# Kernel optimization log

Measured on AMD Instinct MI355X. Metric: run time of the kernel, lower is better.

Reference implementation:

```python
import jax, jax.numpy as jnp
import numpy as np

IN_DIM, HID_DIM, OUT_DIM = 768, 512, 256
B = 1024


def setup_inputs() -> dict:
    key = jax.random.key(0)
    ks = jax.random.split(key, 8)
    s = lambda fan_in: 1.0 / np.sqrt(fan_in)
    return {
        "combin_emb": jax.random.normal(ks[0], (B, IN_DIM), jnp.float32),
        "s_emb": jax.random.normal(ks[1], (B, HID_DIM), jnp.float32),
        # fn1: Linear(hid, hid); torch weight layout [out, in]
        "W1": jax.random.uniform(ks[2], (HID_DIM, HID_DIM), jnp.float32, -s(HID_DIM), s(HID_DIM)),
        "b1": jax.random.uniform(ks[3], (HID_DIM,), jnp.float32, -s(HID_DIM), s(HID_DIM)),
        # fn2: Linear(in, hid)
        "W2": jax.random.uniform(ks[4], (HID_DIM, IN_DIM), jnp.float32, -s(IN_DIM), s(IN_DIM)),
        "b2": jax.random.uniform(ks[5], (HID_DIM,), jnp.float32, -s(IN_DIM), s(IN_DIM)),
        # fn3: Linear(hid, out)
        "W3": jax.random.uniform(ks[6], (OUT_DIM, HID_DIM), jnp.float32, -s(HID_DIM), s(HID_DIM)),
        "b3": jax.random.uniform(ks[7], (OUT_DIM,), jnp.float32, -s(HID_DIM), s(HID_DIM)),
    }


def reference(combin_emb, s_emb, W1, b1, W2, b2, W3, b3):
    scale = 1.0 / np.sqrt(HID_DIM)
    c_emb = combin_emb @ W2.T + b2          # [B, H] query
    t_emb = s_emb @ W1.T + b1               # [B, H] key
    # outer-product scores: [B, H, H], softmax over key axis (last)
    scores = scale * c_emb[:, :, None] * t_emb[:, None, :]
    attn = jax.nn.softmax(scores, axis=-1)
    # value is raw s_emb: [B, H, H] @ [B, H] -> [B, H]
    out = jax.nn.relu(jnp.einsum('bij,bj->bi', attn, s_emb))
    return out @ W3.T + b3                  # [B, OUT]
```

## Files before the change

### kernel.cpp

```cpp
#include <hip/hip_runtime.h>
#include <hip/hip_bf16.h>


#define B_SZ 1024
#define HID 512
#define IN_D 768
#define OUT_D 256
#define NK 8

typedef float floatx16 __attribute__((ext_vector_type(16)));
typedef short short8  __attribute__((ext_vector_type(8)));

__device__ __forceinline__ unsigned pack_bf16(float a, float b) {
    unsigned ua = __float_as_uint(a) + 0x8000u;
    unsigned ub = __float_as_uint(b) + 0x8000u;
    return __builtin_amdgcn_perm(ub, ua, 0x07060302);
}
__device__ __forceinline__ uint4 pack8(float4 lo, float4 hi) {
    uint4 v;
    v.x = pack_bf16(lo.x, lo.y); v.y = pack_bf16(lo.z, lo.w);
    v.z = pack_bf16(hi.x, hi.y); v.w = pack_bf16(hi.z, hi.w);
    return v;
}

template<bool A_BF16>
__device__ __forceinline__ void gemm32_tile(
    const void* Aip, const float* __restrict__ Wp,
    const float* __restrict__ bias, float* __restrict__ C,
    int N, int K, int nch, int row0, int col0,
    uint4 (*stage)[128], float (*redf)[64])
{
    const int tid  = threadIdx.x;
    const int w    = tid >> 6;
    const int lane = tid & 63;
    const int r    = lane >> 1;
    const int h    = lane & 1;
    const int m    = lane & 31;
    const int kh   = lane >> 5;
    const int k0   = w * nch * 16;

    uint4* As = &stage[w][0];
    uint4* Bs = &stage[w][64];
    const uint4* fa = &stage[w][m * 2 + kh];
    const uint4* fb = &stage[w][64 + m * 2 + kh];

    const float* pw = Wp + (size_t)(col0 + r) * K + k0 + h * 8;

    floatx16 acc = {};

    if (A_BF16) {
        const __hip_bfloat16* Ab = (const __hip_bfloat16*)Aip;
        const __hip_bfloat16* pa = Ab + (size_t)(row0 + r) * K + k0 + h * 8;
        uint4 av = *(const uint4*)pa;
        float4 b0 = *(const float4*)pw, b1 = *(const float4*)(pw + 4);
        for (int c = 0; c < nch; ++c) {
            As[lane] = av;
            Bs[lane] = pack8(b0, b1);
            if (c + 1 < nch) {
                pa += 16; pw += 16;
                av = *(const uint4*)pa;
                b0 = *(const float4*)pw; b1 = *(const float4*)(pw + 4);
            }
            uint4 a4 = *fa, b4 = *fb;
            acc = __builtin_amdgcn_mfma_f32_32x32x16_bf16(
                *(short8*)&a4, *(short8*)&b4, acc, 0, 0, 0);
        }
    } else {
        const float* Af = (const float*)Aip;
        const float* pa = Af + (size_t)(row0 + r) * K + k0 + h * 8;
        float4 a0 = *(const float4*)pa, a1 = *(const float4*)(pa + 4);
        float4 b0 = *(const float4*)pw, b1 = *(const float4*)(pw + 4);
        for (int c = 0; c < nch; ++c) {
            As[lane] = pack8(a0, a1);
            Bs[lane] = pack8(b0, b1);
            if (c + 1 < nch) {
                pa += 16; pw += 16;
                a0 = *(const float4*)pa; a1 = *(const float4*)(pa + 4);
                b0 = *(const float4*)pw; b1 = *(const float4*)(pw + 4);
            }
            uint4 a4 = *fa, b4 = *fb;
            acc = __builtin_amdgcn_mfma_f32_32x32x16_bf16(
                *(short8*)&a4, *(short8*)&b4, acc, 0, 0, 0);
        }
    }

    if (w > 0) {
        #pragma unroll
        for (int q = 0; q < 16; ++q) redf[(w - 1) * 16 + q][lane] = acc[q];
    }
    __syncthreads();
    if (w == 0) {
        #pragma unroll
        for (int s = 0; s < 3; ++s)
            #pragma unroll
            for (int q = 0; q < 16; ++q) acc[q] += redf[s * 16 + q][lane];
        const int ccol = col0 + m;
        const float bv = bias[ccol];
        float* cb = C + (size_t)row0 * N + ccol;
        #pragma unroll
        for (int q = 0; q < 16; ++q) {
            int rr = (q & 3) + 8 * (q >> 2) + 4 * kh;
            cb[(size_t)rr * N] = acc[q] + bv;
        }
    }
}

__global__ __launch_bounds__(256) void gemm_ct_k(
    const float* __restrict__ combin, const float* __restrict__ W2,
    const float* __restrict__ b2, float* __restrict__ c_emb,
    const float* __restrict__ s_emb, const float* __restrict__ W1,
    const float* __restrict__ b1, float* __restrict__ t_emb)
{
    __shared__ uint4 stage[4][128];
    __shared__ float redf[48][64];
    int id = blockIdx.x;
    if (id < 512) {
        gemm32_tile<false>(combin, W2, b2, c_emb, HID, IN_D, 12,
                           (id >> 4) * 32, (id & 15) * 32, stage, redf);
    } else {
        id -= 512;
        gemm32_tile<false>(s_emb, W1, b1, t_emb, HID, HID, 8,
                           (id >> 4) * 32, (id & 15) * 32, stage, redf);
    }
}

__global__ __launch_bounds__(256) void gemm_out_k(
    const __hip_bfloat16* __restrict__ o2, const float* __restrict__ W3,
    const float* __restrict__ b3, float* __restrict__ out)
{
    __shared__ uint4 stage[4][128];
    __shared__ float redf[48][64];
    int id = blockIdx.x;
    gemm32_tile<true>(o2, W3, b3, out, OUT_D, HID, 8,
                      (id >> 3) * 32, (id & 7) * 32, stage, redf);
}

__global__ __launch_bounds__(256) void attn_taylor(
    const float* __restrict__ c_emb, const float* __restrict__ t_emb,
    const float* __restrict__ s_emb, unsigned* __restrict__ o2u)
{
    __shared__ float t_s[HID];
    __shared__ float v_s[HID];
    __shared__ float part[256][17];
    __shared__ float red2[16][16];
    __shared__ float fin[16];

    const int b = blockIdx.x, tid = threadIdx.x;

    if (tid < 128) ((float4*)t_s)[tid] = ((const float4*)(t_emb + (size_t)b * HID))[tid];
    else           ((float4*)v_s)[tid - 128] = ((const float4*)(s_emb + (size_t)b * HID))[tid - 128];
    float2 cc = ((const float2*)(c_emb + (size_t)b * HID))[tid];
    __syncthreads();

    float2 tt = ((float2*)t_s)[tid];
    float2 vv = ((float2*)v_s)[tid];
    float tp0 = 1.f, tp1 = 1.f;
    #pragma unroll
    for (int k = 0; k < NK; ++k) {
        part[tid][k]      = tp0 + tp1;
        part[tid][k + NK] = fmaf(tp0, vv.x, tp1 * vv.y);
        tp0 *= tt.x; tp1 *= tt.y;
    }
    __syncthreads();
    {
        int k = tid & 15, g = tid >> 4;
        float s = 0.f;
        #pragma unroll
        for (int r = 0; r < 16; ++r) s += part[g * 16 + r][k];
        red2[g][k] = s;
    }
    __syncthreads();
    if (tid < 16) {
        float s = 0.f;
        #pragma unroll
        for (int g = 0; g < 16; ++g) s += red2[g][tid];
        fin[tid] = s;
    }
    __syncthreads();

    const float invf[NK] = {1.f, 1.f, 0.5f, 1.f / 6.f, 1.f / 24.f,
                            1.f / 120.f, 1.f / 720.f, 1.f / 5040.f};
    float cp[NK], cm[NK];
    #pragma unroll
    for (int k = 0; k < NK; ++k) {
        cp[k] = fin[k] * invf[k];
        cm[k] = fin[k + NK] * invf[k];
    }

    const float scale = 0.04419417382415922f;
    float a0 = scale * cc.x, a1 = scale * cc.y;
    float n0 = cm[NK - 1], d0 = cp[NK - 1], n1 = cm[NK - 1], d1 = cp[NK - 1];
    #pragma unroll
    for (int k = NK - 2; k >= 0; --k) {
        n0 = fmaf(n0, a0, cm[k]); d0 = fmaf(d0, a0, cp[k]);
        n1 = fmaf(n1, a1, cm[k]); d1 = fmaf(d1, a1, cp[k]);
    }
    float r0 = n0 * __builtin_amdgcn_rcpf(d0);
    float r1 = n1 * __builtin_amdgcn_rcpf(d1);
    r0 = r0 > 0.f ? r0 : 0.f;
    r1 = r1 > 0.f ? r1 : 0.f;
    o2u[(size_t)b * (HID / 2) + tid] = pack_bf16(r0, r1);
}

extern "C" void kernel_launch(void* const* d_in, const int* in_sizes, int n_in,
                              void* d_out, int out_size, void* d_ws, size_t ws_size,
                              hipStream_t stream)
{
    const float* combin = (const float*)d_in[0];
    const float* s_emb  = (const float*)d_in[1];
    const float* W1     = (const float*)d_in[2];
    const float* b1     = (const float*)d_in[3];
    const float* W2     = (const float*)d_in[4];
    const float* b2     = (const float*)d_in[5];
    const float* W3     = (const float*)d_in[6];
    const float* b3     = (const float*)d_in[7];
    float* out = (float*)d_out;

    float* ws = (float*)d_ws;
    float* c_emb = ws;
    float* t_emb = ws + (size_t)B_SZ * HID;
    unsigned* o2u = (unsigned*)(ws + (size_t)2 * B_SZ * HID);

    gemm_ct_k<<<1024, 256, 0, stream>>>(combin, W2, b2, c_emb, s_emb, W1, b1, t_emb);
    attn_taylor<<<B_SZ, 256, 0, stream>>>(c_emb, t_emb, s_emb, o2u);
    gemm_out_k<<<256, 256, 0, stream>>>((const __hip_bfloat16*)o2u, W3, b3, out);
}
```

Before: 93.80 us.

## Pre-convert inputs to bf16 and use one-wave-per-tile direct-load MFMA GEMMs

Adds a conversion kernel that turns activations and weights into bf16 buffers up front. The GEMMs then drop LDS staging and the cross-wave split-K reduction: each wavefront computes a full 32x32 tile with fragments loaded straight from global memory. This removes repeated fp32 reads and per-block conversion, shared-memory traffic and the block barrier. The cost is an extra launch plus a full write and reread of the converted data, and fewer blocks: each wave now runs the whole K loop serially with uncoalesced fragment loads.

```diff
diff --git a/kernel.cpp b/kernel.cpp
--- a/kernel.cpp
+++ b/kernel.cpp
@@ -16,123 +16,81 @@
     unsigned ub = __float_as_uint(b) + 0x8000u;
     return __builtin_amdgcn_perm(ub, ua, 0x07060302);
 }
-__device__ __forceinline__ uint4 pack8(float4 lo, float4 hi) {
-    uint4 v;
-    v.x = pack_bf16(lo.x, lo.y); v.y = pack_bf16(lo.z, lo.w);
-    v.z = pack_bf16(hi.x, hi.y); v.w = pack_bf16(hi.z, hi.w);
-    return v;
+
+__global__ __launch_bounds__(256) void tobf16(
+    const float* __restrict__ combin, const float* __restrict__ s_emb,
+    const float* __restrict__ W1, const float* __restrict__ W2,
+    const float* __restrict__ W3,
+    unsigned* __restrict__ combin_h, unsigned* __restrict__ s_emb_h,
+    unsigned* __restrict__ W1_h, unsigned* __restrict__ W2_h,
+    unsigned* __restrict__ W3_h)
+{
+    int p = blockIdx.x * 256 + threadIdx.x;
+    const float* src; unsigned* dst; int off;
+    if      (p < 393216) { src = combin; dst = combin_h; off = p; }
+    else if (p < 655360) { src = s_emb;  dst = s_emb_h;  off = p - 393216; }
+    else if (p < 786432) { src = W1;     dst = W1_h;     off = p - 655360; }
+    else if (p < 983040) { src = W2;     dst = W2_h;     off = p - 786432; }
+    else                 { src = W3;     dst = W3_h;     off = p - 983040; }
+    float2 v = ((const float2*)src)[off];
+    dst[off] = pack_bf16(v.x, v.y);
 }
 
-template<bool A_BF16>
-__device__ __forceinline__ void gemm32_tile(
-    const void* Aip, const float* __restrict__ Wp,
+template<int K>
+__device__ __forceinline__ void tile32_direct(
+    const unsigned short* __restrict__ A, const unsigned short* __restrict__ W,
     const float* __restrict__ bias, float* __restrict__ C,
-    int N, int K, int nch, int row0, int col0,
-    uint4 (*stage)[128], float (*redf)[64])
+    int N, int row0, int col0)
 {
-    const int tid  = threadIdx.x;
-    const int w    = tid >> 6;
-    const int lane = tid & 63;
-    const int r    = lane >> 1;
-    const int h    = lane & 1;
-    const int m    = lane & 31;
-    const int kh   = lane >> 5;
-    const int k0   = w * nch * 16;
+    const int lane = threadIdx.x & 63;
+    const int m  = lane & 31;
+    const int kh = lane >> 5;
 
-    uint4* As = &stage[w][0];
-    uint4* Bs = &stage[w][64];
-    const uint4* fa = &stage[w][m * 2 + kh];
-    const uint4* fb = &stage[w][64 + m * 2 + kh];
-
-    const float* pw = Wp + (size_t)(col0 + r) * K + k0 + h * 8;
+    const uint4* pa = (const uint4*)(A + (size_t)(row0 + m) * K + kh * 8);
+    const uint4* pb = (const uint4*)(W + (size_t)(col0 + m) * K + kh * 8);
 
     floatx16 acc = {};
-
-    if (A_BF16) {
-        const __hip_bfloat16* Ab = (const __hip_bfloat16*)Aip;
-        const __hip_bfloat16* pa = Ab + (size_t)(row0 + r) * K + k0 + h * 8;
-        uint4 av = *(const uint4*)pa;
-        float4 b0 = *(const float4*)pw, b1 = *(const float4*)(pw + 4);
-        for (int c = 0; c < nch; ++c) {
-            As[lane] = av;
-            Bs[lane] = pack8(b0, b1);
-            if (c + 1 < nch) {
-                pa += 16; pw += 16;
-                av = *(const uint4*)pa;
-                b0 = *(const float4*)pw; b1 = *(const float4*)(pw + 4);
-            }
-            uint4 a4 = *fa, b4 = *fb;
-            acc = __builtin_amdgcn_mfma_f32_32x32x16_bf16(
-                *(short8*)&a4, *(short8*)&b4, acc, 0, 0, 0);
-        }
-    } else {
-        const float* Af = (const float*)Aip;
-        const float* pa = Af + (size_t)(row0 + r) * K + k0 + h * 8;
-        float4 a0 = *(const float4*)pa, a1 = *(const float4*)(pa + 4);
-        float4 b0 = *(const float4*)pw, b1 = *(const float4*)(pw + 4);
-        for (int c = 0; c < nch; ++c) {
-            As[lane] = pack8(a0, a1);
-            Bs[lane] = pack8(b0, b1);
-            if (c + 1 < nch) {
-                pa += 16; pw += 16;
-                a0 = *(const float4*)pa; a1 = *(const float4*)(pa + 4);
-                b0 = *(const float4*)pw; b1 = *(const float4*)(pw + 4);
-            }
-            uint4 a4 = *fa, b4 = *fb;
-            acc = __builtin_amdgcn_mfma_f32_32x32x16_bf16(
-                *(short8*)&a4, *(short8*)&b4, acc, 0, 0, 0);
-        }
+    #pragma unroll 8
+    for (int i = 0; i < K / 16; ++i) {
+        uint4 a4 = pa[2 * i];
+        uint4 b4 = pb[2 * i];
+        acc = __builtin_amdgcn_mfma_f32_32x32x16_bf16(
+            *(short8*)&a4, *(short8*)&b4, acc, 0, 0, 0);
     }
 
-    if (w > 0) {
-        #pragma unroll
-        for (int q = 0; q < 16; ++q) redf[(w - 1) * 16 + q][lane] = acc[q];
-    }
-    __syncthreads();
-    if (w == 0) {
-        #pragma unroll
-        for (int s = 0; s < 3; ++s)
-            #pragma unroll
-            for (int q = 0; q < 16; ++q) acc[q] += redf[s * 16 + q][lane];
-        const int ccol = col0 + m;
-        const float bv = bias[ccol];
-        float* cb = C + (size_t)row0 * N + ccol;
-        #pragma unroll
-        for (int q = 0; q < 16; ++q) {
-            int rr = (q & 3) + 8 * (q >> 2) + 4 * kh;
-            cb[(size_t)rr * N] = acc[q] + bv;
-        }
+    const int ccol = col0 + m;
+    const float bv = bias[ccol];
+    float* cb = C + (size_t)row0 * N + ccol;
+    #pragma unroll
+    for (int q = 0; q < 16; ++q) {
+        int rr = (q & 3) + 8 * (q >> 2) + 4 * kh;
+        cb[(size_t)rr * N] = acc[q] + bv;
     }
 }
 
-__global__ __launch_bounds__(256) void gemm_ct_k(
-    const float* __restrict__ combin, const float* __restrict__ W2,
+__global__ __launch_bounds__(256) void gemm_ct_direct(
+    const unsigned short* __restrict__ combin_h, const unsigned short* __restrict__ W2_h,
     const float* __restrict__ b2, float* __restrict__ c_emb,
-    const float* __restrict__ s_emb, const float* __restrict__ W1,
+    const unsigned short* __restrict__ s_emb_h, const unsigned short* __restrict__ W1_h,
     const float* __restrict__ b1, float* __restrict__ t_emb)
 {
-    __shared__ uint4 stage[4][128];
-    __shared__ float redf[48][64];
-    int id = blockIdx.x;
+    int id = blockIdx.x * 4 + (threadIdx.x >> 6);
     if (id < 512) {
-        gemm32_tile<false>(combin, W2, b2, c_emb, HID, IN_D, 12,
-                           (id >> 4) * 32, (id & 15) * 32, stage, redf);
+        tile32_direct<IN_D>(combin_h, W2_h, b2, c_emb, HID,
+                            (id >> 4) * 32, (id & 15) * 32);
     } else {
         id -= 512;
-        gemm32_tile<false>(s_emb, W1, b1, t_emb, HID, HID, 8,
-                           (id >> 4) * 32, (id & 15) * 32, stage, redf);
+        tile32_direct<HID>(s_emb_h, W1_h, b1, t_emb, HID,
+                           (id >> 4) * 32, (id & 15) * 32);
     }
 }
 
-__global__ __launch_bounds__(256) void gemm_out_k(
-    const __hip_bfloat16* __restrict__ o2, const float* __restrict__ W3,
+__global__ __launch_bounds__(256) void gemm_out_direct(
+    const unsigned short* __restrict__ o2h, const unsigned short* __restrict__ W3_h,
     const float* __restrict__ b3, float* __restrict__ out)
 {
-    __shared__ uint4 stage[4][128];
-    __shared__ float redf[48][64];
-    int id = blockIdx.x;
-    gemm32_tile<true>(o2, W3, b3, out, OUT_D, HID, 8,
-                      (id >> 3) * 32, (id & 7) * 32, stage, redf);
+    int id = blockIdx.x * 4 + (threadIdx.x >> 6);
+    tile32_direct<HID>(o2h, W3_h, b3, out, OUT_D, (id >> 3) * 32, (id & 7) * 32);
 }
 
 __global__ __launch_bounds__(256) void attn_taylor(
@@ -219,9 +177,19 @@
     float* ws = (float*)d_ws;
     float* c_emb = ws;
     float* t_emb = ws + (size_t)B_SZ * HID;
-    unsigned* o2u = (unsigned*)(ws + (size_t)2 * B_SZ * HID);
+    unsigned short* h = (unsigned short*)(ws + (size_t)2 * B_SZ * HID);
+    unsigned short* o2h      = h;
+    unsigned short* combin_h = o2h + 524288;
+    unsigned short* s_emb_h  = combin_h + 786432;
+    unsigned short* W1_h     = s_emb_h + 524288;
+    unsigned short* W2_h     = W1_h + 262144;
+    unsigned short* W3_h     = W2_h + 393216;
 
-    gemm_ct_k<<<1024, 256, 0, stream>>>(combin, W2, b2, c_emb, s_emb, W1, b1, t_emb);
-    attn_taylor<<<B_SZ, 256, 0, stream>>>(c_emb, t_emb, s_emb, o2u);
-    gemm_out_k<<<256, 256, 0, stream>>>((const __hip_bfloat16*)o2u, W3, b3, out);
+    tobf16<<<4096, 256, 0, stream>>>(combin, s_emb, W1, W2, W3,
+        (unsigned*)combin_h, (unsigned*)s_emb_h, (unsigned*)W1_h,
+        (unsigned*)W2_h, (unsigned*)W3_h);
+    gemm_ct_direct<<<256, 256, 0, stream>>>(combin_h, W2_h, b2, c_emb,
+                                            s_emb_h, W1_h, b1, t_emb);
+    attn_taylor<<<B_SZ, 256, 0, stream>>>(c_emb, t_emb, s_emb, (unsigned*)o2h);
+    gemm_out_direct<<<64, 256, 0, stream>>>(o2h, W3_h, b3, out);
 }
```

After: 98.76 us. 5.3% more time.

## Fuse three kernels into one persistent kernel with software grid barriers

Applied to the files above, without the earlier changes.

Replaces the three-kernel pipeline (input GEMMs, Taylor attention, output GEMM) with one 512-block kernel that runs each stage in turn, separated by flag-based grid barriers in global memory. A small kernel zeroes the flags first. Each block now does two GEMM tiles and two attention rows, and shared memory is reused across stages through a union. The aim is to remove launch gaps and tail effects between kernels. The risks are the cost of spinning at the barriers, halved block-level parallelism in the first two stages, and deadlock if all 512 blocks cannot be resident at once.

```diff
diff --git a/kernel.cpp b/kernel.cpp
--- a/kernel.cpp
+++ b/kernel.cpp
@@ -7,6 +7,7 @@
 #define IN_D 768
 #define OUT_D 256
 #define NK 8
+#define NBLK 512
 
 typedef float floatx16 __attribute__((ext_vector_type(16)));
 typedef short short8  __attribute__((ext_vector_type(8)));
@@ -22,6 +23,12 @@
     v.z = pack_bf16(hi.x, hi.y); v.w = pack_bf16(hi.z, hi.w);
     return v;
 }
+
+union SharedMem {
+    struct { uint4 stage[4][128]; float redf[48][64]; } g;
+    struct { float t_s[HID]; float v_s[HID]; float part[256][17];
+             float red2[16][16]; float fin[16]; } a;
+};
 
 template<bool A_BF16>
 __device__ __forceinline__ void gemm32_tile(
@@ -49,8 +56,8 @@
     floatx16 acc = {};
 
     if (A_BF16) {
-        const __hip_bfloat16* Ab = (const __hip_bfloat16*)Aip;
-        const __hip_bfloat16* pa = Ab + (size_t)(row0 + r) * K + k0 + h * 8;
+        const unsigned short* Ab = (const unsigned short*)Aip;
+        const unsigned short* pa = Ab + (size_t)(row0 + r) * K + k0 + h * 8;
         uint4 av = *(const uint4*)pa;
         float4 b0 = *(const float4*)pw, b1 = *(const float4*)(pw + 4);
         for (int c = 0; c < nch; ++c) {
@@ -105,60 +112,24 @@
     }
 }
 
-__global__ __launch_bounds__(256) void gemm_ct_k(
-    const float* __restrict__ combin, const float* __restrict__ W2,
-    const float* __restrict__ b2, float* __restrict__ c_emb,
-    const float* __restrict__ s_emb, const float* __restrict__ W1,
-    const float* __restrict__ b1, float* __restrict__ t_emb)
-{
-    __shared__ uint4 stage[4][128];
-    __shared__ float redf[48][64];
-    int id = blockIdx.x;
-    if (id < 512) {
-        gemm32_tile<false>(combin, W2, b2, c_emb, HID, IN_D, 12,
-                           (id >> 4) * 32, (id & 15) * 32, stage, redf);
-    } else {
-        id -= 512;
-        gemm32_tile<false>(s_emb, W1, b1, t_emb, HID, HID, 8,
-                           (id >> 4) * 32, (id & 15) * 32, stage, redf);
-    }
-}
-
-__global__ __launch_bounds__(256) void gemm_out_k(
-    const __hip_bfloat16* __restrict__ o2, const float* __restrict__ W3,
-    const float* __restrict__ b3, float* __restrict__ out)
-{
-    __shared__ uint4 stage[4][128];
-    __shared__ float redf[48][64];
-    int id = blockIdx.x;
-    gemm32_tile<true>(o2, W3, b3, out, OUT_D, HID, 8,
-                      (id >> 3) * 32, (id & 7) * 32, stage, redf);
-}
-
-__global__ __launch_bounds__(256) void attn_taylor(
-    const float* __restrict__ c_emb, const float* __restrict__ t_emb,
-    const float* __restrict__ s_emb, unsigned* __restrict__ o2u)
-{
-    __shared__ float t_s[HID];
-    __shared__ float v_s[HID];
-    __shared__ float part[256][17];
-    __shared__ float red2[16][16];
-    __shared__ float fin[16];
-
-    const int b = blockIdx.x, tid = threadIdx.x;
-
-    if (tid < 128) ((float4*)t_s)[tid] = ((const float4*)(t_emb + (size_t)b * HID))[tid];
-    else           ((float4*)v_s)[tid - 128] = ((const float4*)(s_emb + (size_t)b * HID))[tid - 128];
+__device__ __forceinline__ void attn_one(
+    int b, const float* __restrict__ c_emb, const float* __restrict__ t_emb,
+    const float* __restrict__ s_emb, unsigned* __restrict__ o2u, SharedMem* sm)
+{
+    const int tid = threadIdx.x;
+
+    if (tid < 128) ((float4*)sm->a.t_s)[tid] = ((const float4*)(t_emb + (size_t)b * HID))[tid];
+    else           ((float4*)sm->a.v_s)[tid - 128] = ((const float4*)(s_emb + (size_t)b * HID))[tid - 128];
     float2 cc = ((const float2*)(c_emb + (size_t)b * HID))[tid];
     __syncthreads();
 
-    float2 tt = ((float2*)t_s)[tid];
-    float2 vv = ((float2*)v_s)[tid];
+    float2 tt = ((float2*)sm->a.t_s)[tid];
+    float2 vv = ((float2*)sm->a.v_s)[tid];
     float tp0 = 1.f, tp1 = 1.f;
     #pragma unroll
     for (int k = 0; k < NK; ++k) {
-        part[tid][k]      = tp0 + tp1;
-        part[tid][k + NK] = fmaf(tp0, vv.x, tp1 * vv.y);
+        sm->a.part[tid][k]      = tp0 + tp1;
+        sm->a.part[tid][k + NK] = fmaf(tp0, vv.x, tp1 * vv.y);
         tp0 *= tt.x; tp1 *= tt.y;
     }
     __syncthreads();
@@ -166,15 +137,15 @@
         int k = tid & 15, g = tid >> 4;
         float s = 0.f;
         #pragma unroll
-        for (int r = 0; r < 16; ++r) s += part[g * 16 + r][k];
-        red2[g][k] = s;
+        for (int r = 0; r < 16; ++r) s += sm->a.part[g * 16 + r][k];
+        sm->a.red2[g][k] = s;
     }
     __syncthreads();
     if (tid < 16) {
         float s = 0.f;
         #pragma unroll
-        for (int g = 0; g < 16; ++g) s += red2[g][tid];
-        fin[tid] = s;
+        for (int g = 0; g < 16; ++g) s += sm->a.red2[g][tid];
+        sm->a.fin[tid] = s;
     }
     __syncthreads();
 
@@ -183,8 +154,8 @@
     float cp[NK], cm[NK];
     #pragma unroll
     for (int k = 0; k < NK; ++k) {
-        cp[k] = fin[k] * invf[k];
-        cm[k] = fin[k + NK] * invf[k];
+        cp[k] = sm->a.fin[k] * invf[k];
+        cm[k] = sm->a.fin[k + NK] * invf[k];
     }
 
     const float scale = 0.04419417382415922f;
@@ -200,6 +171,60 @@
     r0 = r0 > 0.f ? r0 : 0.f;
     r1 = r1 > 0.f ? r1 : 0.f;
     o2u[(size_t)b * (HID / 2) + tid] = pack_bf16(r0, r1);
+}
+
+__device__ __forceinline__ void grid_barrier(unsigned* flags, unsigned sv)
+{
+    __syncthreads();
+    __threadfence();
+    if (threadIdx.x == 0)
+        __hip_atomic_store(flags + blockIdx.x, sv, __ATOMIC_RELAXED,
+                           __HIP_MEMORY_SCOPE_AGENT);
+    if (threadIdx.x < 64) {
+        for (int i = threadIdx.x; i < NBLK; i += 64) {
+            while (__hip_atomic_load(flags + i, __ATOMIC_RELAXED,
+                                     __HIP_MEMORY_SCOPE_AGENT) < sv) { }
+        }
+    }
+    __threadfence();
+    __syncthreads();
+}
+
+__global__ __launch_bounds__(512) void zero_flags(unsigned* flags)
+{
+    flags[threadIdx.x] = 0u;
+}
+
+__global__ __launch_bounds__(256, 2) void fused_all(
+    const float* __restrict__ combin, const float* __restrict__ s_emb,
+    const float* __restrict__ W1, const float* __restrict__ b1,
+    const float* __restrict__ W2, const float* __restrict__ b2,
+    const float* __restrict__ W3, const float* __restrict__ b3,
+    float* __restrict__ c_emb, float* __restrict__ t_emb,
+    unsigned* __restrict__ o2u, unsigned* __restrict__ flags,
+    float* __restrict__ out)
+{
+    __shared__ SharedMem sm;
+    const int g = blockIdx.x;
+
+    gemm32_tile<false>(combin, W2, b2, c_emb, HID, IN_D, 12,
+                       (g >> 4) * 32, (g & 15) * 32, sm.g.stage, sm.g.redf);
+    __syncthreads();
+    gemm32_tile<false>(s_emb, W1, b1, t_emb, HID, HID, 8,
+                       (g >> 4) * 32, (g & 15) * 32, sm.g.stage, sm.g.redf);
+
+    grid_barrier(flags, 1u);
+
+    attn_one(2 * g,     c_emb, t_emb, s_emb, o2u, &sm);
+    __syncthreads();
+    attn_one(2 * g + 1, c_emb, t_emb, s_emb, o2u, &sm);
+
+    grid_barrier(flags, 2u);
+
+    if (g < 256) {
+        gemm32_tile<true>(o2u, W3, b3, out, OUT_D, HID, 8,
+                          (g >> 3) * 32, (g & 7) * 32, sm.g.stage, sm.g.redf);
+    }
 }
 
 extern "C" void kernel_launch(void* const* d_in, const int* in_sizes, int n_in,
@@ -217,11 +242,12 @@
     float* out = (float*)d_out;
 
     float* ws = (float*)d_ws;
-    float* c_emb = ws;
-    float* t_emb = ws + (size_t)B_SZ * HID;
-    unsigned* o2u = (unsigned*)(ws + (size_t)2 * B_SZ * HID);
-
-    gemm_ct_k<<<1024, 256, 0, stream>>>(combin, W2, b2, c_emb, s_emb, W1, b1, t_emb);
-    attn_taylor<<<B_SZ, 256, 0, stream>>>(c_emb, t_emb, s_emb, o2u);
-    gemm_out_k<<<256, 256, 0, stream>>>((const __hip_bfloat16*)o2u, W3, b3, out);
-}
+    float*    c_emb = ws;
+    float*    t_emb = ws + (size_t)B_SZ * HID;
+    unsigned* o2u   = (unsigned*)(ws + (size_t)2 * B_SZ * HID);
+    unsigned* flags = o2u + (size_t)B_SZ * HID / 2;
+
+    zero_flags<<<1, NBLK, 0, stream>>>(flags);
+    fused_all<<<NBLK, 256, 0, stream>>>(combin, s_emb, W1, b1, W2, b2, W3, b3,
+                                        c_emb, t_emb, o2u, flags, out);
+}
```

Result: slower. 238.5 us (+154.3%).
